# Kernel optimization log

Hardware: AMD Instinct MI355X
Metric: run time of the kernel (lower is better)

The kernel has to match this reference:

```python
import jax, jax.numpy as jnp
import numpy as np

IN_FEATURES = 256
OUT_FEATURES = 256


def setup_inputs() -> dict:
    key = jax.random.key(0)
    kx, kw, ks, kb = jax.random.split(key, 4)
    x = jax.random.normal(kx, (131072, IN_FEATURES), dtype=jnp.float32)
    # Xavier-uniform init for the latent fp weight [out, in]
    limit = float(np.sqrt(6.0 / (IN_FEATURES + OUT_FEATURES)))
    W = jax.random.uniform(kw, (OUT_FEATURES, IN_FEATURES), dtype=jnp.float32,
                           minval=-limit, maxval=limit)
    # scale initialized to ones in the module; perturb slightly to make it non-trivial
    scale = jnp.ones((OUT_FEATURES,), dtype=jnp.float32) + 0.01 * jax.random.normal(ks, (OUT_FEATURES,), dtype=jnp.float32)
    bias = 0.01 * jax.random.normal(kb, (OUT_FEATURES,), dtype=jnp.float32)
    return {"x": x, "W": W, "scale": scale, "bias": bias}


def reference(x, W, scale, bias):
    # STE binarization: forward value is sign(W), gradient passes through to W
    binary_w = W + jax.lax.stop_gradient(jnp.sign(W) - W)          # [out, in]
    scaled_w = binary_w * scale[:, None]                           # per-output-channel rescale
    # F.linear(x, scaled_w, bias) = x @ scaled_w.T + bias
    return jnp.einsum('bi,oi->bo', x, scaled_w) + bias
```

## Files before the change

### kernel.cpp

```cpp
#include <hip/hip_runtime.h>
#include <hip/hip_bf16.h>


typedef __bf16 bf16_t;
typedef __attribute__((ext_vector_type(8))) __bf16 bf16x8;
typedef __attribute__((ext_vector_type(4))) float f32x4;
typedef __attribute__((ext_vector_type(4))) short s16x4;

#define MROWS 131072
#define NDIM 256
#define KDIM 256
#define BM 64

__global__ __launch_bounds__(256) void prep_w_kernel(const float* __restrict__ W,
                                                     bf16_t* __restrict__ wb) {
    int idx = blockIdx.x * 256 + threadIdx.x;
    float w = W[idx];
    float v = (w > 0.0f) ? 1.0f : ((w < 0.0f) ? -1.0f : 0.0f);
    wb[idx] = (bf16_t)v;
}

__global__ __launch_bounds__(256) void bin_gemm_kernel(
        const float* __restrict__ x,
        const bf16_t* __restrict__ wb,
        const float* __restrict__ scale,
        const float* __restrict__ bias,
        float* __restrict__ out) {
    __shared__ __align__(16) char Alds[BM * KDIM * 2];

    const int tid   = threadIdx.x;
    const int lane  = tid & 63;
    const int wave  = tid >> 6;
    const int mbase = blockIdx.x * BM;

    const float* xt = x + (size_t)mbase * KDIM;
    #pragma unroll
    for (int i = 0; i < 16; ++i) {
        int q    = i * 256 + tid;
        int row  = q >> 6;
        int colq = q & 63;
        f32x4 v = *reinterpret_cast<const f32x4*>(xt + (size_t)q * 4);
        bf16_t b0 = (bf16_t)v.x, b1 = (bf16_t)v.y, b2 = (bf16_t)v.z, b3 = (bf16_t)v.w;
        s16x4 b;
        b.x = *reinterpret_cast<short*>(&b0);
        b.y = *reinterpret_cast<short*>(&b1);
        b.z = *reinterpret_cast<short*>(&b2);
        b.w = *reinterpret_cast<short*>(&b3);
        int boff = row * 512 + ((colq * 8) ^ ((row & 7) << 4));
        *reinterpret_cast<s16x4*>(Alds + boff) = b;
    }
    __syncthreads();

    const int obase = wave * 64;
    const int lrow  = lane & 15;
    const int lk    = lane >> 4;

    f32x4 acc[4][4] = {};

    #pragma unroll
    for (int ks = 0; ks < 8; ++ks) {
        bf16x8 a[4], b[4];
        #pragma unroll
        for (int mi = 0; mi < 4; ++mi) {
            int row  = mi * 16 + lrow;
            int cb   = ks * 64 + lk * 16;
            int boff = row * 512 + (cb ^ ((row & 7) << 4));
            a[mi] = *reinterpret_cast<const bf16x8*>(Alds + boff);
        }
        #pragma unroll
        for (int ni = 0; ni < 4; ++ni) {
            int orow = obase + ni * 16 + lrow;
            const bf16_t* p = wb + (size_t)orow * KDIM + ks * 32 + lk * 8;
            b[ni] = *reinterpret_cast<const bf16x8*>(p);
        }
        #pragma unroll
        for (int mi = 0; mi < 4; ++mi)
            #pragma unroll
            for (int ni = 0; ni < 4; ++ni)
                acc[mi][ni] = __builtin_amdgcn_mfma_f32_16x16x32_bf16(
                                  a[mi], b[ni], acc[mi][ni], 0, 0, 0);
    }

    float sc[4], bi[4];
    #pragma unroll
    for (int ni = 0; ni < 4; ++ni) {
        int col = obase + ni * 16 + lrow;
        sc[ni] = scale[col];
        bi[ni] = bias[col];
    }
    #pragma unroll
    for (int mi = 0; mi < 4; ++mi) {
        #pragma unroll
        for (int ni = 0; ni < 4; ++ni) {
            int col = obase + ni * 16 + lrow;
            #pragma unroll
            for (int r = 0; r < 4; ++r) {
                int row = mbase + mi * 16 + lk * 4 + r;
                out[(size_t)row * NDIM + col] = acc[mi][ni][r] * sc[ni] + bi[ni];
            }
        }
    }
}

extern "C" void kernel_launch(void* const* d_in, const int* in_sizes, int n_in,
                              void* d_out, int out_size, void* d_ws, size_t ws_size,
                              hipStream_t stream) {
    const float* x     = (const float*)d_in[0];
    const float* W     = (const float*)d_in[1];
    const float* scale = (const float*)d_in[2];
    const float* bias  = (const float*)d_in[3];
    float*       out   = (float*)d_out;
    bf16_t*      wb    = (bf16_t*)d_ws;

    prep_w_kernel<<<NDIM * KDIM / 256, 256, 0, stream>>>(W, wb);
    bin_gemm_kernel<<<MROWS / BM, 256, 0, stream>>>(x, wb, scale, bias, out);
}
```

Measured before the change: 268.2 us.

## Load x tiles directly from global into registers, drop LDS staging

Removes the shared-memory staging of the x tile: each wave now loads its A fragments straight from global memory as fp32 and converts them to bf16 in registers, eliminating the LDS writes, reads and the barrier. The output stores are also made nontemporal to avoid polluting cache. The trade-off is that all four waves re-read the same x rows from global/L2 (4x redundant loads), relying on cache hits instead of LDS reuse.

Result: slower. 299.6 us (+11.7%).

```diff
diff --git a/kernel.cpp b/kernel.cpp
--- a/kernel.cpp
+++ b/kernel.cpp
@@ -5,7 +5,6 @@
 typedef __bf16 bf16_t;
 typedef __attribute__((ext_vector_type(8))) __bf16 bf16x8;
 typedef __attribute__((ext_vector_type(4))) float f32x4;
-typedef __attribute__((ext_vector_type(4))) short s16x4;
 
 #define MROWS 131072
 #define NDIM 256
@@ -20,40 +19,26 @@
     wb[idx] = (bf16_t)v;
 }
 
+__device__ inline bf16x8 cvt8(f32x4 lo, f32x4 hi) {
+    bf16x8 r;
+    r[0] = (bf16_t)lo.x; r[1] = (bf16_t)lo.y; r[2] = (bf16_t)lo.z; r[3] = (bf16_t)lo.w;
+    r[4] = (bf16_t)hi.x; r[5] = (bf16_t)hi.y; r[6] = (bf16_t)hi.z; r[7] = (bf16_t)hi.w;
+    return r;
+}
+
 __global__ __launch_bounds__(256) void bin_gemm_kernel(
         const float* __restrict__ x,
         const bf16_t* __restrict__ wb,
         const float* __restrict__ scale,
         const float* __restrict__ bias,
         float* __restrict__ out) {
-    __shared__ __align__(16) char Alds[BM * KDIM * 2];
-
     const int tid   = threadIdx.x;
     const int lane  = tid & 63;
     const int wave  = tid >> 6;
     const int mbase = blockIdx.x * BM;
-
-    const float* xt = x + (size_t)mbase * KDIM;
-    #pragma unroll
-    for (int i = 0; i < 16; ++i) {
-        int q    = i * 256 + tid;
-        int row  = q >> 6;
-        int colq = q & 63;
-        f32x4 v = *reinterpret_cast<const f32x4*>(xt + (size_t)q * 4);
-        bf16_t b0 = (bf16_t)v.x, b1 = (bf16_t)v.y, b2 = (bf16_t)v.z, b3 = (bf16_t)v.w;
-        s16x4 b;
-        b.x = *reinterpret_cast<short*>(&b0);
-        b.y = *reinterpret_cast<short*>(&b1);
-        b.z = *reinterpret_cast<short*>(&b2);
-        b.w = *reinterpret_cast<short*>(&b3);
-        int boff = row * 512 + ((colq * 8) ^ ((row & 7) << 4));
-        *reinterpret_cast<s16x4*>(Alds + boff) = b;
-    }
-    __syncthreads();
-
-    const int obase = wave * 64;
     const int lrow  = lane & 15;
     const int lk    = lane >> 4;
+    const int obase = wave * 64;
 
     f32x4 acc[4][4] = {};
 
@@ -62,16 +47,15 @@
         bf16x8 a[4], b[4];
         #pragma unroll
         for (int mi = 0; mi < 4; ++mi) {
-            int row  = mi * 16 + lrow;
-            int cb   = ks * 64 + lk * 16;
-            int boff = row * 512 + (cb ^ ((row & 7) << 4));
-            a[mi] = *reinterpret_cast<const bf16x8*>(Alds + boff);
+            const float* pa = x + (size_t)(mbase + mi * 16 + lrow) * KDIM + ks * 32 + lk * 8;
+            f32x4 lo = *reinterpret_cast<const f32x4*>(pa);
+            f32x4 hi = *reinterpret_cast<const f32x4*>(pa + 4);
+            a[mi] = cvt8(lo, hi);
         }
         #pragma unroll
         for (int ni = 0; ni < 4; ++ni) {
-            int orow = obase + ni * 16 + lrow;
-            const bf16_t* p = wb + (size_t)orow * KDIM + ks * 32 + lk * 8;
-            b[ni] = *reinterpret_cast<const bf16x8*>(p);
+            const bf16_t* pb = wb + (size_t)(obase + ni * 16 + lrow) * KDIM + ks * 32 + lk * 8;
+            b[ni] = *reinterpret_cast<const bf16x8*>(pb);
         }
         #pragma unroll
         for (int mi = 0; mi < 4; ++mi)
@@ -96,7 +80,8 @@
             #pragma unroll
             for (int r = 0; r < 4; ++r) {
                 int row = mbase + mi * 16 + lk * 4 + r;
-                out[(size_t)row * NDIM + col] = acc[mi][ni][r] * sc[ni] + bi[ni];
+                __builtin_nontemporal_store(acc[mi][ni][r] * sc[ni] + bi[ni],
+                                            out + (size_t)row * NDIM + col);
             }
         }
     }
```
